# Kernel optimization log

Hardware: AMD Instinct MI355X
Metric: run time of the kernel (lower is better)

## Reference

```python
import jax, jax.numpy as jnp
import numpy as np


def setup_inputs() -> dict:
    key = jax.random.key(0)
    k1, k2, k3 = jax.random.split(key, 3)
    B, S, D = 2, 2048, 4096
    x = jax.random.normal(k1, (B, S, D), dtype=jnp.float32)
    weight = jax.random.normal(k2, (D, D), dtype=jnp.float32)  # [out, in]
    bias = jax.random.normal(k3, (D,), dtype=jnp.float32)
    return {"x": x, "weight": weight, "bias": bias}


def reference(x, weight, bias):
    # STE binarization: forward uses sign(W) (sign(0)=0, matching torch.sign)
    w = jnp.sign(weight)
    # F.linear: x @ w.T + b
    return jnp.einsum('bsk,nk->bsn', x, w) + bias
```

## Files before the change

### kernel.cpp

```cpp
#include <hip/hip_runtime.h>
#include <hip/hip_bf16.h>
#include <stdint.h>

#define M_DIM 4096
#define N_DIM 4096
#define K_DIM 4096
#define NT 128

typedef float f32x4 __attribute__((ext_vector_type(4)));
typedef __bf16 bf16x8 __attribute__((ext_vector_type(8)));
typedef float f4 __attribute__((ext_vector_type(4)));
typedef unsigned int u32x4 __attribute__((ext_vector_type(4)));
typedef unsigned short u16x4 __attribute__((ext_vector_type(4)));

__device__ __forceinline__ uint16_t f32_to_bf16_rn(float f) {
  uint32_t u = __float_as_uint(f);
  u += 0x7fffu + ((u >> 16) & 1u);
  return (uint16_t)(u >> 16);
}

__global__ void convert_w_kernel(const u32x4* __restrict__ w4,
                                 u16x4* __restrict__ s4, int n4) {
  int idx = blockIdx.x * blockDim.x + threadIdx.x;
  int stride = gridDim.x * blockDim.x;
  for (int i = idx; i < n4; i += stride) {
    u32x4 v = w4[i];
    u16x4 o;
#pragma unroll
    for (int j = 0; j < 4; ++j) {
      uint32_t b = v[j];
      o[j] = ((b & 0x7fffffffu) == 0u)
                 ? (uint16_t)0
                 : (uint16_t)(0x3F80u | ((b >> 16) & 0x8000u));
    }
    s4[i] = o;
  }
}

__global__ void convert_x_kernel(const f4* __restrict__ x4,
                                 uint16_t* __restrict__ Ab, int n4) {
  int idx = blockIdx.x * blockDim.x + threadIdx.x;
  int stride = gridDim.x * blockDim.x;
  for (int i = idx; i < n4; i += stride) {
    f4 v = x4[i];
    u16x4 h, l;
#pragma unroll
    for (int j = 0; j < 4; ++j) {
      uint16_t hb = f32_to_bf16_rn(v[j]);
      float r = v[j] - __uint_as_float((uint32_t)hb << 16);
      h[j] = hb;
      l[j] = f32_to_bf16_rn(r);
    }
    int flat = i * 4;
    int m = flat >> 12;
    int k = flat & 4095;
    *(u16x4*)&Ab[(size_t)m * 8192 + k] = h;
    *(u16x4*)&Ab[(size_t)m * 8192 + 4096 + k] = l;
  }
}

__device__ __forceinline__ void gload_lds16(const void* g, void* l) {
  __builtin_amdgcn_global_load_lds(
      (__attribute__((address_space(1))) void*)(g),
      (__attribute__((address_space(3))) void*)(l),
      16, 0, 0);
}

__global__ __launch_bounds__(512, 2)
void bingemm8(const uint16_t* __restrict__ Ab, const uint16_t* __restrict__ Bs,
              const float* __restrict__ bias, float* __restrict__ out) {
  __shared__ uint16_t sA[2][2][8192];
  __shared__ uint16_t sB[2][2][8192];

  const int t = threadIdx.x;
  const int lane = t & 63;
  const int w = t >> 6;
  const int r15 = lane & 15;

  const int bid = blockIdx.x;
  const int swz = (bid & 7) * 32 + (bid >> 3);
  const int bm = (swz >> 4) * 256;
  const int bn = (swz & 15) * 256;

  const int srow = t >> 3;
  const int scol = (((t & 7) ^ (srow & 7)) * 8);
  const size_t aThr = (size_t)(bm + srow) * 8192 + scol;
  const size_t bThr = (size_t)(bn + srow) * 4096 + scol;

#define STAGE_A(KT, HH, BUF)                                        \
  do {                                                              \
    const uint16_t* g = Ab + aThr + (size_t)(HH) * 128 * 8192 +     \
                        (size_t)(KT) * 64;                          \
    gload_lds16(g, &sA[BUF][HH][t * 8]);                            \
    gload_lds16(g + (size_t)64 * 8192, &sA[BUF][HH][t * 8 + 4096]); \
  } while (0)
#define STAGE_B(KT, HH, BUF)                                        \
  do {                                                              \
    const uint16_t* g = Bs + bThr + (size_t)(HH) * 128 * 4096 +     \
                        (size_t)((KT) & 63) * 64;                   \
    gload_lds16(g, &sB[BUF][HH][t * 8]);                            \
    gload_lds16(g + (size_t)64 * 4096, &sB[BUF][HH][t * 8 + 4096]); \
  } while (0)

  const int klane = lane >> 4;
  const int cb0 = (klane * 16) ^ ((lane & 7) << 4);
  const int whA = w >> 2;
  const int whB = (w & 3) >> 1;
  const int wcl = (w & 1) * 64;
  const int eA0 = r15 * 64 + (cb0 >> 1);
  const int eA1 = eA0 ^ 32;
  const int eB0 = (wcl + r15) * 64 + (cb0 >> 1);
  const int eB1 = eB0 ^ 32;

  bf16x8 rA[4][2], rB[4][2];
  f32x4 acc[8][4];
#pragma unroll
  for (int m = 0; m < 8; ++m)
#pragma unroll
    for (int n = 0; n < 4; ++n) acc[m][n] = (f32x4){0.f, 0.f, 0.f, 0.f};

#define LOAD_A(BUF, MOFF)                                            \
  {                                                                  \
    _Pragma("unroll") for (int m = 0; m < 4; ++m) {                  \
      rA[m][0] = *(const bf16x8*)&sA[BUF][whA][eA0 + ((MOFF) + m) * 1024]; \
      rA[m][1] = *(const bf16x8*)&sA[BUF][whA][eA1 + ((MOFF) + m) * 1024]; \
    }                                                                \
  }
#define LOAD_B(BUF, NB)                                              \
  {                                                                  \
    _Pragma("unroll") for (int n = 0; n < 2; ++n) {                  \
      rB[(NB) + n][0] = *(const bf16x8*)&sB[BUF][whB][eB0 + ((NB) + n) * 1024]; \
      rB[(NB) + n][1] = *(const bf16x8*)&sB[BUF][whB][eB1 + ((NB) + n) * 1024]; \
    }                                                                \
  }
#define MFMA_Q(MB, NB)                                               \
  {                                                                  \
    _Pragma("unroll") for (int mm = 0; mm < 4; ++mm)                 \
    _Pragma("unroll") for (int nn = 0; nn < 2; ++nn)                 \
    _Pragma("unroll") for (int ks = 0; ks < 2; ++ks)                 \
      acc[(MB) + mm][(NB) + nn] = __builtin_amdgcn_mfma_f32_16x16x32_bf16( \
          rA[mm][ks], rB[(NB) + nn][ks], acc[(MB) + mm][(NB) + nn], 0, 0, 0); \
  }
#define PH_PRE()                                        \
  __builtin_amdgcn_s_barrier();                         \
  asm volatile("s_waitcnt lgkmcnt(0)" ::: "memory");    \
  __builtin_amdgcn_sched_barrier(0);                    \
  __builtin_amdgcn_s_setprio(1);
#define PH_POST()                                       \
  __builtin_amdgcn_s_setprio(0);                        \
  __builtin_amdgcn_s_barrier();
#define PH_POST_VM()                                    \
  __builtin_amdgcn_s_setprio(0);                        \
  asm volatile("s_waitcnt vmcnt(4)" ::: "memory");      \
  __builtin_amdgcn_s_barrier();

  STAGE_B(0, 0, 0);
  STAGE_A(0, 0, 0);
  STAGE_B(0, 1, 0);
  STAGE_A(0, 1, 0);
  STAGE_B(1, 0, 1);
  STAGE_A(1, 0, 1);
  asm volatile("s_waitcnt vmcnt(4)" ::: "memory");
  __builtin_amdgcn_s_barrier();

  for (int i = 0; i < NT / 2; ++i) {
    const int t1 = 2 * i + 1;
    const int tp0 = (2 * i + 2 < NT) ? (2 * i + 2) : (NT - 1);
    const int tp1 = (2 * i + 3 < NT) ? (2 * i + 3) : (NT - 1);
    LOAD_A(0, 0);
    LOAD_B(0, 0);
    STAGE_B(t1, 1, 1);
    PH_PRE();
    MFMA_Q(0, 0);
    PH_POST();
    LOAD_B(0, 2);
    STAGE_A(t1, 1, 1);
    PH_PRE();
    MFMA_Q(0, 2);
    PH_POST();
    LOAD_A(0, 4);
    STAGE_B(tp0, 0, 0);
    PH_PRE();
    MFMA_Q(4, 2);
    PH_POST();
    STAGE_A(tp0, 0, 0);
    PH_PRE();
    MFMA_Q(4, 0);
    PH_POST_VM();
    LOAD_A(1, 0);
    LOAD_B(1, 0);
    STAGE_B(tp0, 1, 0);
    PH_PRE();
    MFMA_Q(0, 0);
    PH_POST();
    LOAD_B(1, 2);
    STAGE_A(tp0, 1, 0);
    PH_PRE();
    MFMA_Q(0, 2);
    PH_POST();
    LOAD_A(1, 4);
    STAGE_B(tp1, 0, 1);
    PH_PRE();
    MFMA_Q(4, 2);
    PH_POST();
    STAGE_A(tp1, 0, 1);
    PH_PRE();
    MFMA_Q(4, 0);
    PH_POST_VM();
  }

  asm volatile("s_waitcnt vmcnt(0)" ::: "memory");

  const int rowg = (lane >> 4) * 4;
#pragma unroll
  for (int n = 0; n < 4; ++n) {
    const int col = bn + (w & 3) * 64 + n * 16 + r15;
    const float bv = bias[col];
#pragma unroll
    for (int m = 0; m < 8; ++m) {
      const int row0 = bm + (w >> 2) * 128 + m * 16 + rowg;
#pragma unroll
      for (int k = 0; k < 4; ++k)
        out[(size_t)(row0 + k) * N_DIM + col] = acc[m][n][k] + bv;
    }
  }
}

__global__ void fallback_gemm(const float* __restrict__ x,
                              const float* __restrict__ w,
                              const float* __restrict__ bias,
                              float* __restrict__ out) {
  __shared__ float sx[16][17];
  __shared__ float sw[16][17];
  int tx = threadIdx.x & 15, ty = threadIdx.x >> 4;
  int m = blockIdx.y * 16 + ty;
  int n = blockIdx.x * 16 + tx;
  float acc = 0.f;
  for (int k0 = 0; k0 < K_DIM; k0 += 16) {
    sx[ty][tx] = x[(size_t)m * K_DIM + k0 + tx];
    float wv = w[(size_t)(blockIdx.x * 16 + ty) * K_DIM + k0 + tx];
    sw[ty][tx] = (wv > 0.f) ? 1.f : ((wv < 0.f) ? -1.f : 0.f);
    __syncthreads();
#pragma unroll
    for (int kk = 0; kk < 16; ++kk) acc += sx[ty][kk] * sw[tx][kk];
    __syncthreads();
  }
  out[(size_t)m * N_DIM + n] = acc + bias[n];
}

extern "C" void kernel_launch(void* const* d_in, const int* in_sizes, int n_in,
                              void* d_out, int out_size, void* d_ws,
                              size_t ws_size, hipStream_t stream) {
  const float* x = (const float*)d_in[0];
  const float* w = (const float*)d_in[1];
  const float* bias = (const float*)d_in[2];
  float* out = (float*)d_out;

  const size_t elems = (size_t)N_DIM * K_DIM;
  const size_t need = elems * 2u * 3u;

  if (ws_size < need) {
    dim3 grid(N_DIM / 16, M_DIM / 16);
    fallback_gemm<<<grid, 256, 0, stream>>>(x, w, bias, out);
    return;
  }

  uint16_t* Sb = (uint16_t*)d_ws;
  uint16_t* Ab = Sb + elems;

  const int n4 = (int)(elems / 4);
  convert_w_kernel<<<4096, 256, 0, stream>>>((const u32x4*)w, (u16x4*)Sb, n4);
  convert_x_kernel<<<4096, 256, 0, stream>>>((const f4*)x, Ab, n4);

  bingemm8<<<dim3(256), 512, 0, stream>>>(Ab, Sb, bias, out);
}
```

Before: 402.8 us.

## Split MFMA phases by k-half and reorder staging of A/B halves

Restructures the 8-phase main loop so each phase computes a 4x4 MFMA block over one k-half instead of a 4x2 block over both k-halves. Register fragments are split into per-k-half arrays, and all B fragments are loaded together per k-half. Global-to-LDS staging is reordered so A halves are staged for the current buffer early and B halves for the next tile later. The goal is to cut LDS fragment reloads and change the overlap between loads and MFMA. It risks violating the buffer-readiness assumptions behind the vmcnt(4) waits and needs careful correctness checking.

```diff
diff --git a/kernel.cpp b/kernel.cpp
--- a/kernel.cpp
+++ b/kernel.cpp
@@ -112,34 +112,39 @@
   const int eB0 = (wcl + r15) * 64 + (cb0 >> 1);
   const int eB1 = eB0 ^ 32;
 
-  bf16x8 rA[4][2], rB[4][2];
+  bf16x8 rAa[4], rAb[4], rBa[4], rBb[4];
   f32x4 acc[8][4];
 #pragma unroll
   for (int m = 0; m < 8; ++m)
 #pragma unroll
     for (int n = 0; n < 4; ++n) acc[m][n] = (f32x4){0.f, 0.f, 0.f, 0.f};
 
-#define LOAD_A(BUF, MOFF)                                            \
-  {                                                                  \
-    _Pragma("unroll") for (int m = 0; m < 4; ++m) {                  \
-      rA[m][0] = *(const bf16x8*)&sA[BUF][whA][eA0 + ((MOFF) + m) * 1024]; \
-      rA[m][1] = *(const bf16x8*)&sA[BUF][whA][eA1 + ((MOFF) + m) * 1024]; \
-    }                                                                \
-  }
-#define LOAD_B(BUF, NB)                                              \
-  {                                                                  \
-    _Pragma("unroll") for (int n = 0; n < 2; ++n) {                  \
-      rB[(NB) + n][0] = *(const bf16x8*)&sB[BUF][whB][eB0 + ((NB) + n) * 1024]; \
-      rB[(NB) + n][1] = *(const bf16x8*)&sB[BUF][whB][eB1 + ((NB) + n) * 1024]; \
-    }                                                                \
-  }
-#define MFMA_Q(MB, NB)                                               \
-  {                                                                  \
-    _Pragma("unroll") for (int mm = 0; mm < 4; ++mm)                 \
-    _Pragma("unroll") for (int nn = 0; nn < 2; ++nn)                 \
-    _Pragma("unroll") for (int ks = 0; ks < 2; ++ks)                 \
-      acc[(MB) + mm][(NB) + nn] = __builtin_amdgcn_mfma_f32_16x16x32_bf16( \
-          rA[mm][ks], rB[(NB) + nn][ks], acc[(MB) + mm][(NB) + nn], 0, 0, 0); \
+#define LOAD_A0(BUF, MOFF)                                                 \
+  {                                                                        \
+    _Pragma("unroll") for (int m = 0; m < 4; ++m)                          \
+        rAa[m] = *(const bf16x8*)&sA[BUF][whA][eA0 + ((MOFF) + m) * 1024]; \
+  }
+#define LOAD_A1(BUF, MOFF)                                                 \
+  {                                                                        \
+    _Pragma("unroll") for (int m = 0; m < 4; ++m)                          \
+        rAb[m] = *(const bf16x8*)&sA[BUF][whA][eA1 + ((MOFF) + m) * 1024]; \
+  }
+#define LOAD_B0(BUF)                                                       \
+  {                                                                        \
+    _Pragma("unroll") for (int n = 0; n < 4; ++n)                          \
+        rBa[n] = *(const bf16x8*)&sB[BUF][whB][eB0 + n * 1024];            \
+  }
+#define LOAD_B1(BUF)                                                       \
+  {                                                                        \
+    _Pragma("unroll") for (int n = 0; n < 4; ++n)                          \
+        rBb[n] = *(const bf16x8*)&sB[BUF][whB][eB1 + n * 1024];            \
+  }
+#define MFMA16(MB, RA, RB)                                                 \
+  {                                                                        \
+    _Pragma("unroll") for (int mm = 0; mm < 4; ++mm)                       \
+    _Pragma("unroll") for (int nn = 0; nn < 4; ++nn)                       \
+        acc[(MB) + mm][nn] = __builtin_amdgcn_mfma_f32_16x16x32_bf16(      \
+            RA[mm], RB[nn], acc[(MB) + mm][nn], 0, 0, 0);                  \
   }
 #define PH_PRE()                                        \
   __builtin_amdgcn_s_barrier();                         \
@@ -155,11 +160,11 @@
   __builtin_amdgcn_s_barrier();
 
   STAGE_B(0, 0, 0);
+  STAGE_B(0, 1, 0);
   STAGE_A(0, 0, 0);
-  STAGE_B(0, 1, 0);
   STAGE_A(0, 1, 0);
   STAGE_B(1, 0, 1);
-  STAGE_A(1, 0, 1);
+  STAGE_B(1, 1, 1);
   asm volatile("s_waitcnt vmcnt(4)" ::: "memory");
   __builtin_amdgcn_s_barrier();
 
@@ -167,45 +172,49 @@
     const int t1 = 2 * i + 1;
     const int tp0 = (2 * i + 2 < NT) ? (2 * i + 2) : (NT - 1);
     const int tp1 = (2 * i + 3 < NT) ? (2 * i + 3) : (NT - 1);
-    LOAD_A(0, 0);
-    LOAD_B(0, 0);
-    STAGE_B(t1, 1, 1);
-    PH_PRE();
-    MFMA_Q(0, 0);
-    PH_POST();
-    LOAD_B(0, 2);
+    LOAD_A0(0, 0);
+    LOAD_B0(0);
+    STAGE_A(t1, 0, 1);
+    PH_PRE();
+    MFMA16(0, rAa, rBa);
+    PH_POST();
+    LOAD_A1(0, 0);
+    LOAD_B1(0);
     STAGE_A(t1, 1, 1);
     PH_PRE();
-    MFMA_Q(0, 2);
-    PH_POST();
-    LOAD_A(0, 4);
+    MFMA16(0, rAb, rBb);
+    PH_POST();
+    LOAD_A0(0, 4);
     STAGE_B(tp0, 0, 0);
     PH_PRE();
-    MFMA_Q(4, 2);
-    PH_POST();
+    MFMA16(4, rAa, rBa);
+    PH_POST();
+    LOAD_A1(0, 4);
+    STAGE_B(tp0, 1, 0);
+    PH_PRE();
+    MFMA16(4, rAb, rBb);
+    PH_POST_VM();
+    LOAD_A0(1, 0);
+    LOAD_B0(1);
     STAGE_A(tp0, 0, 0);
     PH_PRE();
-    MFMA_Q(4, 0);
-    PH_POST_VM();
-    LOAD_A(1, 0);
-    LOAD_B(1, 0);
-    STAGE_B(tp0, 1, 0);
-    PH_PRE();
-    MFMA_Q(0, 0);
-    PH_POST();
-    LOAD_B(1, 2);
+    MFMA16(0, rAa, rBa);
+    PH_POST();
+    LOAD_A1(1, 0);
+    LOAD_B1(1);
     STAGE_A(tp0, 1, 0);
     PH_PRE();
-    MFMA_Q(0, 2);
-    PH_POST();
-    LOAD_A(1, 4);
+    MFMA16(0, rAb, rBb);
+    PH_POST();
+    LOAD_A0(1, 4);
     STAGE_B(tp1, 0, 1);
     PH_PRE();
-    MFMA_Q(4, 2);
-    PH_POST();
-    STAGE_A(tp1, 0, 1);
-    PH_PRE();
-    MFMA_Q(4, 0);
+    MFMA16(4, rAa, rBa);
+    PH_POST();
+    LOAD_A1(1, 4);
+    STAGE_B(tp1, 1, 1);
+    PH_PRE();
+    MFMA16(4, rAb, rBb);
     PH_POST_VM();
   }
 
```

Result: faster. 379.5 us (-5.8%).

## Reuse B tile across hi/lo A halves and fuse conversion kernels

Applied to the files above, without the earlier changes.

The GEMM now splits the A operand into separate hi and lo LDS buffers and iterates over the 64 real K tiles, loading each B tile once and applying it to both the hi and lo halves of A. Previously B was reloaded for each half of the doubled K range. This halves B global traffic and B LDS reads. The two conversion kernels are merged into one launch with 8-wide vector loads and stores. The pipeline changes from prefetching a full tile ahead to staging pieces within the tile, with vmcnt(0) waits that may expose more load latency.

```diff
diff --git a/kernel.cpp b/kernel.cpp
--- a/kernel.cpp
+++ b/kernel.cpp
@@ -5,13 +5,13 @@
 #define M_DIM 4096
 #define N_DIM 4096
 #define K_DIM 4096
-#define NT 128
+#define NTO 64
 
 typedef float f32x4 __attribute__((ext_vector_type(4)));
 typedef __bf16 bf16x8 __attribute__((ext_vector_type(8)));
 typedef float f4 __attribute__((ext_vector_type(4)));
 typedef unsigned int u32x4 __attribute__((ext_vector_type(4)));
-typedef unsigned short u16x4 __attribute__((ext_vector_type(4)));
+typedef unsigned short u16x8 __attribute__((ext_vector_type(8)));
 
 __device__ __forceinline__ uint16_t f32_to_bf16_rn(float f) {
   uint32_t u = __float_as_uint(f);
@@ -19,43 +19,50 @@
   return (uint16_t)(u >> 16);
 }
 
-__global__ void convert_w_kernel(const u32x4* __restrict__ w4,
-                                 u16x4* __restrict__ s4, int n4) {
-  int idx = blockIdx.x * blockDim.x + threadIdx.x;
-  int stride = gridDim.x * blockDim.x;
-  for (int i = idx; i < n4; i += stride) {
-    u32x4 v = w4[i];
-    u16x4 o;
-#pragma unroll
-    for (int j = 0; j < 4; ++j) {
-      uint32_t b = v[j];
-      o[j] = ((b & 0x7fffffffu) == 0u)
-                 ? (uint16_t)0
-                 : (uint16_t)(0x3F80u | ((b >> 16) & 0x8000u));
+__global__ void convert_fused(const u32x4* __restrict__ w4,
+                              u16x8* __restrict__ s8,
+                              const f4* __restrict__ x4,
+                              uint16_t* __restrict__ Ab, int n8) {
+  const int half = 2048;
+  if (blockIdx.x < half) {
+    int idx = blockIdx.x * 256 + threadIdx.x;
+    int stride = half * 256;
+    for (int i = idx; i < n8; i += stride) {
+      u32x4 a = w4[2 * i], b = w4[2 * i + 1];
+      u16x8 o;
+#pragma unroll
+      for (int j = 0; j < 4; ++j) {
+        uint32_t ua = a[j], ub = b[j];
+        o[j] = ((ua & 0x7fffffffu) == 0u)
+                   ? (uint16_t)0
+                   : (uint16_t)(0x3F80u | ((ua >> 16) & 0x8000u));
+        o[4 + j] = ((ub & 0x7fffffffu) == 0u)
+                       ? (uint16_t)0
+                       : (uint16_t)(0x3F80u | ((ub >> 16) & 0x8000u));
+      }
+      s8[i] = o;
     }
-    s4[i] = o;
-  }
-}
-
-__global__ void convert_x_kernel(const f4* __restrict__ x4,
-                                 uint16_t* __restrict__ Ab, int n4) {
-  int idx = blockIdx.x * blockDim.x + threadIdx.x;
-  int stride = gridDim.x * blockDim.x;
-  for (int i = idx; i < n4; i += stride) {
-    f4 v = x4[i];
-    u16x4 h, l;
-#pragma unroll
-    for (int j = 0; j < 4; ++j) {
-      uint16_t hb = f32_to_bf16_rn(v[j]);
-      float r = v[j] - __uint_as_float((uint32_t)hb << 16);
-      h[j] = hb;
-      l[j] = f32_to_bf16_rn(r);
+  } else {
+    int idx = (blockIdx.x - half) * 256 + threadIdx.x;
+    int stride = half * 256;
+    for (int i = idx; i < n8; i += stride) {
+      f4 a = x4[2 * i], b = x4[2 * i + 1];
+      u16x8 h, l;
+#pragma unroll
+      for (int j = 0; j < 4; ++j) {
+        uint16_t hb = f32_to_bf16_rn(a[j]);
+        h[j] = hb;
+        l[j] = f32_to_bf16_rn(a[j] - __uint_as_float((uint32_t)hb << 16));
+        uint16_t hb2 = f32_to_bf16_rn(b[j]);
+        h[4 + j] = hb2;
+        l[4 + j] = f32_to_bf16_rn(b[j] - __uint_as_float((uint32_t)hb2 << 16));
+      }
+      int flat = i * 8;
+      int m = flat >> 12;
+      int k = flat & 4095;
+      *(u16x8*)&Ab[(size_t)m * 8192 + k] = h;
+      *(u16x8*)&Ab[(size_t)m * 8192 + 4096 + k] = l;
     }
-    int flat = i * 4;
-    int m = flat >> 12;
-    int k = flat & 4095;
-    *(u16x4*)&Ab[(size_t)m * 8192 + k] = h;
-    *(u16x4*)&Ab[(size_t)m * 8192 + 4096 + k] = l;
   }
 }
 
@@ -69,7 +76,8 @@
 __global__ __launch_bounds__(512, 2)
 void bingemm8(const uint16_t* __restrict__ Ab, const uint16_t* __restrict__ Bs,
               const float* __restrict__ bias, float* __restrict__ out) {
-  __shared__ uint16_t sA[2][2][8192];
+  __shared__ uint16_t sAh[2][8192];
+  __shared__ uint16_t sAl[2][8192];
   __shared__ uint16_t sB[2][2][8192];
 
   const int t = threadIdx.x;
@@ -87,17 +95,24 @@
   const size_t aThr = (size_t)(bm + srow) * 8192 + scol;
   const size_t bThr = (size_t)(bn + srow) * 4096 + scol;
 
-#define STAGE_A(KT, HH, BUF)                                        \
+#define STAGE_AH(KT, HH)                                            \
   do {                                                              \
     const uint16_t* g = Ab + aThr + (size_t)(HH) * 128 * 8192 +     \
                         (size_t)(KT) * 64;                          \
-    gload_lds16(g, &sA[BUF][HH][t * 8]);                            \
-    gload_lds16(g + (size_t)64 * 8192, &sA[BUF][HH][t * 8 + 4096]); \
+    gload_lds16(g, &sAh[HH][t * 8]);                                \
+    gload_lds16(g + (size_t)64 * 8192, &sAh[HH][t * 8 + 4096]);     \
+  } while (0)
+#define STAGE_AL(KT, HH)                                            \
+  do {                                                              \
+    const uint16_t* g = Ab + aThr + (size_t)(HH) * 128 * 8192 +     \
+                        4096 + (size_t)(KT) * 64;                   \
+    gload_lds16(g, &sAl[HH][t * 8]);                                \
+    gload_lds16(g + (size_t)64 * 8192, &sAl[HH][t * 8 + 4096]);     \
   } while (0)
 #define STAGE_B(KT, HH, BUF)                                        \
   do {                                                              \
     const uint16_t* g = Bs + bThr + (size_t)(HH) * 128 * 4096 +     \
-                        (size_t)((KT) & 63) * 64;                   \
+                        (size_t)(KT) * 64;                          \
     gload_lds16(g, &sB[BUF][HH][t * 8]);                            \
     gload_lds16(g + (size_t)64 * 4096, &sB[BUF][HH][t * 8 + 4096]); \
   } while (0)
@@ -112,34 +127,39 @@
   const int eB0 = (wcl + r15) * 64 + (cb0 >> 1);
   const int eB1 = eB0 ^ 32;
 
-  bf16x8 rA[4][2], rB[4][2];
+  bf16x8 rAa[4], rAb[4], rBa[4], rBb[4];
   f32x4 acc[8][4];
 #pragma unroll
   for (int m = 0; m < 8; ++m)
 #pragma unroll
     for (int n = 0; n < 4; ++n) acc[m][n] = (f32x4){0.f, 0.f, 0.f, 0.f};
 
-#define LOAD_A(BUF, MOFF)                                            \
-  {                                                                  \
-    _Pragma("unroll") for (int m = 0; m < 4; ++m) {                  \
-      rA[m][0] = *(const bf16x8*)&sA[BUF][whA][eA0 + ((MOFF) + m) * 1024]; \
-      rA[m][1] = *(const bf16x8*)&sA[BUF][whA][eA1 + ((MOFF) + m) * 1024]; \
-    }                                                                \
-  }
-#define LOAD_B(BUF, NB)                                              \
-  {                                                                  \
-    _Pragma("unroll") for (int n = 0; n < 2; ++n) {                  \
-      rB[(NB) + n][0] = *(const bf16x8*)&sB[BUF][whB][eB0 + ((NB) + n) * 1024]; \
-      rB[(NB) + n][1] = *(const bf16x8*)&sB[BUF][whB][eB1 + ((NB) + n) * 1024]; \
-    }                                                                \
-  }
-#define MFMA_Q(MB, NB)                                               \
-  {                                                                  \
-    _Pragma("unroll") for (int mm = 0; mm < 4; ++mm)                 \
-    _Pragma("unroll") for (int nn = 0; nn < 2; ++nn)                 \
-    _Pragma("unroll") for (int ks = 0; ks < 2; ++ks)                 \
-      acc[(MB) + mm][(NB) + nn] = __builtin_amdgcn_mfma_f32_16x16x32_bf16( \
-          rA[mm][ks], rB[(NB) + nn][ks], acc[(MB) + mm][(NB) + nn], 0, 0, 0); \
+#define LOAD_A0(SRC, MOFF)                                                  \
+  {                                                                         \
+    _Pragma("unroll") for (int m = 0; m < 4; ++m)                           \
+        rAa[m] = *(const bf16x8*)&SRC[whA][eA0 + ((MOFF) + m) * 1024];      \
+  }
+#define LOAD_A1(SRC, MOFF)                                                  \
+  {                                                                         \
+    _Pragma("unroll") for (int m = 0; m < 4; ++m)                           \
+        rAb[m] = *(const bf16x8*)&SRC[whA][eA1 + ((MOFF) + m) * 1024];      \
+  }
+#define LOAD_B0(BUF)                                                        \
+  {                                                                         \
+    _Pragma("unroll") for (int n = 0; n < 4; ++n)                           \
+        rBa[n] = *(const bf16x8*)&sB[BUF][whB][eB0 + n * 1024];             \
+  }
+#define LOAD_B1(BUF)                                                        \
+  {                                                                         \
+    _Pragma("unroll") for (int n = 0; n < 4; ++n)                           \
+        rBb[n] = *(const bf16x8*)&sB[BUF][whB][eB1 + n * 1024];             \
+  }
+#define MFMA16(MB, RA, RB)                                                  \
+  {                                                                         \
+    _Pragma("unroll") for (int mm = 0; mm < 4; ++mm)                        \
+    _Pragma("unroll") for (int nn = 0; nn < 4; ++nn)                        \
+        acc[(MB) + mm][nn] = __builtin_amdgcn_mfma_f32_16x16x32_bf16(       \
+            RA[mm], RB[nn], acc[(MB) + mm][nn], 0, 0, 0);                   \
   }
 #define PH_PRE()                                        \
   __builtin_amdgcn_s_barrier();                         \
@@ -149,64 +169,72 @@
 #define PH_POST()                                       \
   __builtin_amdgcn_s_setprio(0);                        \
   __builtin_amdgcn_s_barrier();
-#define PH_POST_VM()                                    \
+#define PH_POST_VM4()                                   \
   __builtin_amdgcn_s_setprio(0);                        \
   asm volatile("s_waitcnt vmcnt(4)" ::: "memory");      \
   __builtin_amdgcn_s_barrier();
-
+#define PH_POST_VM0()                                   \
+  __builtin_amdgcn_s_setprio(0);                        \
+  asm volatile("s_waitcnt vmcnt(0)" ::: "memory");      \
+  __builtin_amdgcn_s_barrier();
+
+#define TILE_BODY(KT)                                           \
+  {                                                             \
+    const int b = (KT) & 1;                                     \
+    const int bn1 = b ^ 1;                                      \
+    const int kp1 = ((KT) + 1 < NTO) ? ((KT) + 1) : (NTO - 1);  \
+    LOAD_A0(sAh, 0);                                            \
+    LOAD_B0(b);                                                 \
+    STAGE_AL(KT, 0);                                            \
+    PH_PRE();                                                   \
+    MFMA16(0, rAa, rBa);                                        \
+    PH_POST();                                                  \
+    LOAD_A1(sAh, 0);                                            \
+    LOAD_B1(b);                                                 \
+    STAGE_AL(KT, 1);                                            \
+    PH_PRE();                                                   \
+    MFMA16(0, rAb, rBb);                                        \
+    PH_POST();                                                  \
+    LOAD_A0(sAh, 4);                                            \
+    STAGE_B(kp1, 0, bn1);                                       \
+    PH_PRE();                                                   \
+    MFMA16(4, rAa, rBa);                                        \
+    PH_POST();                                                  \
+    LOAD_A1(sAh, 4);                                            \
+    STAGE_B(kp1, 1, bn1);                                       \
+    PH_PRE();                                                   \
+    MFMA16(4, rAb, rBb);                                        \
+    PH_POST_VM4();                                              \
+    LOAD_A0(sAl, 0);                                            \
+    STAGE_AH(kp1, 0);                                           \
+    PH_PRE();                                                   \
+    MFMA16(0, rAa, rBa);                                        \
+    PH_POST();                                                  \
+    LOAD_A1(sAl, 0);                                            \
+    STAGE_AH(kp1, 1);                                           \
+    PH_PRE();                                                   \
+    MFMA16(0, rAb, rBb);                                        \
+    PH_POST();                                                  \
+    LOAD_A0(sAl, 4);                                            \
+    PH_PRE();                                                   \
+    MFMA16(4, rAa, rBa);                                        \
+    PH_POST();                                                  \
+    LOAD_A1(sAl, 4);                                            \
+    PH_PRE();                                                   \
+    MFMA16(4, rAb, rBb);                                        \
+    PH_POST_VM0();                                              \
+  }
+
+  STAGE_AH(0, 0);
+  STAGE_AH(0, 1);
   STAGE_B(0, 0, 0);
-  STAGE_A(0, 0, 0);
   STAGE_B(0, 1, 0);
-  STAGE_A(0, 1, 0);
-  STAGE_B(1, 0, 1);
-  STAGE_A(1, 0, 1);
-  asm volatile("s_waitcnt vmcnt(4)" ::: "memory");
+  asm volatile("s_waitcnt vmcnt(0)" ::: "memory");
   __builtin_amdgcn_s_barrier();
 
-  for (int i = 0; i < NT / 2; ++i) {
-    const int t1 = 2 * i + 1;
-    const int tp0 = (2 * i + 2 < NT) ? (2 * i + 2) : (NT - 1);
-    const int tp1 = (2 * i + 3 < NT) ? (2 * i + 3) : (NT - 1);
-    LOAD_A(0, 0);
-    LOAD_B(0, 0);
-    STAGE_B(t1, 1, 1);
-    PH_PRE();
-    MFMA_Q(0, 0);
-    PH_POST();
-    LOAD_B(0, 2);
-    STAGE_A(t1, 1, 1);
-    PH_PRE();
-    MFMA_Q(0, 2);
-    PH_POST();
-    LOAD_A(0, 4);
-    STAGE_B(tp0, 0, 0);
-    PH_PRE();
-    MFMA_Q(4, 2);
-    PH_POST();
-    STAGE_A(tp0, 0, 0);
-    PH_PRE();
-    MFMA_Q(4, 0);
-    PH_POST_VM();
-    LOAD_A(1, 0);
-    LOAD_B(1, 0);
-    STAGE_B(tp0, 1, 0);
-    PH_PRE();
-    MFMA_Q(0, 0);
-    PH_POST();
-    LOAD_B(1, 2);
-    STAGE_A(tp0, 1, 0);
-    PH_PRE();
-    MFMA_Q(0, 2);
-    PH_POST();
-    LOAD_A(1, 4);
-    STAGE_B(tp1, 0, 1);
-    PH_PRE();
-    MFMA_Q(4, 2);
-    PH_POST();
-    STAGE_A(tp1, 0, 1);
-    PH_PRE();
-    MFMA_Q(4, 0);
-    PH_POST_VM();
+  for (int i2 = 0; i2 < NTO / 2; ++i2) {
+    TILE_BODY(2 * i2);
+    TILE_BODY(2 * i2 + 1);
   }
 
   asm volatile("s_waitcnt vmcnt(0)" ::: "memory");
@@ -268,9 +296,9 @@
   uint16_t* Sb = (uint16_t*)d_ws;
   uint16_t* Ab = Sb + elems;
 
-  const int n4 = (int)(elems / 4);
-  convert_w_kernel<<<4096, 256, 0, stream>>>((const u32x4*)w, (u16x4*)Sb, n4);
-  convert_x_kernel<<<4096, 256, 0, stream>>>((const f4*)x, Ab, n4);
+  const int n8 = (int)(elems / 8);
+  convert_fused<<<4096, 256, 0, stream>>>((const u32x4*)w, (u16x8*)Sb,
+                                          (const f4*)x, Ab, n8);
 
   bingemm8<<<dim3(256), 512, 0, stream>>>(Ab, Sb, bias, out);
 }
```

Result: faster. 390.1 us (-3.2%).
